# Optimization experiments

Measured on AMD Instinct MI355X. Metric: run time of the kernel, lower is better.

The kernel has to match this reference:

```python
import jax, jax.numpy as jnp
import numpy as np

B, L, CIN, COUT, HEADS = 8, 2048, 256, 256, 4
HD = COUT // HEADS
NEG_SLOPE = 0.2


def setup_inputs() -> dict:
    key = jax.random.key(0)
    k1, k2, k3, k4, k5 = jax.random.split(key, 5)
    x = jax.random.normal(k1, (B, L, CIN), dtype=jnp.float32)
    adj_mask = jax.random.randint(k2, (B, L, L), 0, 2) > 0  # bool [B,L,L]
    W = jax.random.normal(k3, (COUT, CIN), dtype=jnp.float32) * (1.0 / np.sqrt(CIN))
    att_src = jax.random.normal(k4, (1, HEADS, 1, HD), dtype=jnp.float32) * 0.1
    att_dst = jax.random.normal(k5, (1, HEADS, 1, HD), dtype=jnp.float32) * 0.1
    return {"x": x, "adj_mask": adj_mask, "W": W, "att_src": att_src, "att_dst": att_dst}


def reference(x, adj_mask, W, att_src, att_dst):
    Bb, Ll, _ = x.shape
    # linear projection (no bias), split heads: [B, H, L, D]
    h = jnp.einsum('blc,oc->blo', x, W).reshape(Bb, Ll, HEADS, HD).transpose(0, 2, 1, 3)
    # additive GAT scores
    a_src = jnp.sum(h * att_src, axis=-1, keepdims=True)          # [B,H,L,1]
    a_dst = jnp.sum(h * att_dst, axis=-1, keepdims=True)          # [B,H,L,1]
    e = a_src + jnp.swapaxes(a_dst, 2, 3)                          # [B,H,L,L]
    e = jnp.where(e >= 0, e, NEG_SLOPE * e)                        # leaky relu
    fill = jnp.finfo(e.dtype).min
    e = jnp.where(adj_mask[:, None, :, :], e, fill)                # mask non-edges
    alpha = jax.nn.softmax(e, axis=-1)                             # [B,H,L,L]
    # dropout is identity in eval/reference mode
    out = jnp.einsum('bhij,bhjd->bhid', alpha, h)                  # [B,H,L,D]
    return out.transpose(0, 2, 1, 3).reshape(Bb, Ll, COUT)
```

## Files before the change

kernel.cpp:

```cpp
#include <hip/hip_runtime.h>

#define B_ 8
#define L_ 2048
#define CIN_ 256
#define COUT_ 256
#define HEADS_ 4
#define HD_ 64
#define NEG_SLOPE_ 0.2f
#define LOG2E_ 1.4426950408889634f

#define TI 32
#define TJ 64
#define NJT (L_ / TJ)

typedef __attribute__((ext_vector_type(4))) float f32x4;
typedef __attribute__((ext_vector_type(8))) __bf16 bf16x8;
typedef __attribute__((ext_vector_type(4))) __bf16 bf16x4;


__global__ __launch_bounds__(256, 2)
void proj_kernel(const float* __restrict__ x, const float* __restrict__ W,
                 const float* __restrict__ att_src, const float* __restrict__ att_dst,
                 const int* __restrict__ adj, unsigned long long* __restrict__ abitsT,
                 __bf16* __restrict__ hF, float2* __restrict__ aE,
                 float2* __restrict__ aF) {
  __shared__ __align__(16) __bf16 Wl[COUT_][80];
  __shared__ __align__(16) __bf16 Al[2][2][512];

  const int tid = threadIdx.x;
  const int r0 = blockIdx.x * TI;
  const int b  = r0 >> 11;
  const int l0 = r0 & (L_ - 1);

  const int w = tid >> 6, lane = tid & 63, col = lane & 15, q = lane >> 4;
  const int si = tid >> 3, soct = tid & 7;
  const int wn = tid >> 2, wkq = tid & 3;

  {
    const size_t wid0 = (size_t)blockIdx.x * 256 + (size_t)w * 64;
    for (int c = 0; c < 64; ++c) {
      const size_t wid = wid0 + c;
      const int* p = adj + wid * 256 + lane;
      unsigned long long b0 = __ballot(p[0]   != 0);
      unsigned long long b1 = __ballot(p[64]  != 0);
      unsigned long long b2 = __ballot(p[128] != 0);
      unsigned long long b3 = __ballot(p[192] != 0);
      if (lane == 0) {
        const size_t row = wid >> 3;
        const int jw0 = (int)(wid & 7) * 4;
        const size_t bb = row >> 11, l = row & 2047;
        unsigned long long* dst = abitsT + (bb << 16) + l;
        dst[(size_t)(jw0 + 0) << 11] = b0;
        dst[(size_t)(jw0 + 1) << 11] = b1;
        dst[(size_t)(jw0 + 2) << 11] = b2;
        dst[(size_t)(jw0 + 3) << 11] = b3;
      }
    }
  }

  f32x4 acc[2][4];
#pragma unroll
  for (int mt = 0; mt < 2; ++mt)
#pragma unroll
    for (int nt = 0; nt < 4; ++nt) acc[mt][nt] = (f32x4)0.f;

  for (int kc = 0; kc < CIN_ / 64; ++kc) {
    __syncthreads();
#pragma unroll
    for (int rg = 0; rg < 4; ++rg) {
      const int row = rg * 64 + wn;
      const float4* ws = (const float4*)(W + (size_t)row * CIN_ + kc * 64 + wkq * 16);
#pragma unroll
      for (int u = 0; u < 4; ++u) {
        float4 f = ws[u];
        bf16x4 v;
        v[0] = (__bf16)f.x; v[1] = (__bf16)f.y; v[2] = (__bf16)f.z; v[3] = (__bf16)f.w;
        *(bf16x4*)&Wl[row][wkq * 16 + u * 4] = v;
      }
    }
    {
      const float4* xs = (const float4*)(x + (size_t)(r0 + si) * CIN_ + kc * 64 + soct * 8);
      float4 f0 = xs[0], f1 = xs[1];
      bf16x8 v;
      v[0] = (__bf16)f0.x; v[1] = (__bf16)f0.y; v[2] = (__bf16)f0.z; v[3] = (__bf16)f0.w;
      v[4] = (__bf16)f1.x; v[5] = (__bf16)f1.y; v[6] = (__bf16)f1.z; v[7] = (__bf16)f1.w;
      *(bf16x8*)&Al[si >> 4][soct >> 2][(((soct & 3) << 4) + (si & 15)) << 3] = v;
    }
    __syncthreads();

    bf16x8 af[2][2], bfr[2][4];
#pragma unroll
    for (int mt = 0; mt < 2; ++mt)
#pragma unroll
      for (int kt = 0; kt < 2; ++kt)
        af[mt][kt] = *(const bf16x8*)&Al[mt][kt][lane << 3];
#pragma unroll
    for (int kt = 0; kt < 2; ++kt)
#pragma unroll
      for (int nt = 0; nt < 4; ++nt)
        bfr[kt][nt] = *(const bf16x8*)&Wl[w * 64 + nt * 16 + col][kt * 32 + q * 8];
#pragma unroll
    for (int kt = 0; kt < 2; ++kt)
#pragma unroll
      for (int mt = 0; mt < 2; ++mt)
#pragma unroll
        for (int nt = 0; nt < 4; ++nt)
          acc[mt][nt] = __builtin_amdgcn_mfma_f32_16x16x32_bf16(
              af[mt][kt], bfr[kt][nt], acc[mt][nt], 0, 0, 0);
  }

  float asv[4], adv[4];
#pragma unroll
  for (int nt = 0; nt < 4; ++nt) {
    asv[nt] = att_src[w * 64 + nt * 16 + col];
    adv[nt] = att_dst[w * 64 + nt * 16 + col];
  }
#pragma unroll
  for (int mt = 0; mt < 2; ++mt)
#pragma unroll
    for (int reg = 0; reg < 4; ++reg) {
      float s = 0.f, d = 0.f;
#pragma unroll
      for (int nt = 0; nt < 4; ++nt) {
        s = fmaf(acc[mt][nt][reg], asv[nt], s);
        d = fmaf(acc[mt][nt][reg], adv[nt], d);
      }
      s += __shfl_xor(s, 1, 64); d += __shfl_xor(d, 1, 64);
      s += __shfl_xor(s, 2, 64); d += __shfl_xor(d, 2, 64);
      s += __shfl_xor(s, 4, 64); d += __shfl_xor(d, 4, 64);
      s += __shfl_xor(s, 8, 64); d += __shfl_xor(d, 8, 64);
      if (col == 0) {
        int il = mt * 16 + q * 4 + reg;
        const size_t idx = ((size_t)(b * HEADS_ + w) << 11) + l0 + il;
        float2 ev, fv;
        ev.x = __builtin_exp2f(s * LOG2E_);
        ev.y = __builtin_exp2f(s * (LOG2E_ * NEG_SLOPE_));
        fv.x = __builtin_exp2f(d * LOG2E_);
        fv.y = __builtin_exp2f(d * (LOG2E_ * NEG_SLOPE_));
        aE[idx] = ev;
        aF[idx] = fv;
      }
    }

  {
    const int jt_p = l0 >> 6;
    const int kt_p = (l0 >> 5) & 1;
    const int qhi = q >> 1, qlo = q & 1;
#pragma unroll
    for (int mt = 0; mt < 2; ++mt) {
      const int qp = mt * 2 + qhi;
#pragma unroll
      for (int nt = 0; nt < 4; ++nt) {
        bf16x4 v;
        v[0] = (__bf16)acc[mt][nt][0];
        v[1] = (__bf16)acc[mt][nt][1];
        v[2] = (__bf16)acc[mt][nt][2];
        v[3] = (__bf16)acc[mt][nt][3];
        const size_t off =
            ((((size_t)(b * HEADS_ + w) * 32 + jt_p) * 2 + kt_p) * 4 + nt) * 512 +
            (qp * 16 + col) * 8 + qlo * 4;
        *(bf16x4*)(hF + off) = v;
      }
    }
  }
}

__global__ __launch_bounds__(512, 4)
void attn_kernel(const __bf16* __restrict__ hF, const float2* __restrict__ aE,
                 const float2* __restrict__ aF,
                 const unsigned long long* __restrict__ abitsT,
                 float* __restrict__ out) {
  __shared__ __align__(16) float comb[HEADS_][64][40];

  const int tid = threadIdx.x;
  const int b  = blockIdx.x & 7;
  const int i0 = (blockIdx.x >> 3) * 32;

  const int w = tid >> 6, lane = tid & 63, col = lane & 15, q = lane >> 4;
  const int hh = w & 3;
  const int jh = w >> 2;
  const int jt0 = jh * (NJT / 2), jt1 = jt0 + NJT / 2;

  const size_t hl = (size_t)(b * HEADS_ + hh);
  const float2 EE[2] = {aE[(hl << 11) + i0 + col],
                        aE[(hl << 11) + i0 + 16 + col]};
  const float* afb = (const float*)(aF + (hl << 11)) + q * 16;
  const __bf16* hb = hF + hl * 131072 + lane * 8;
  const unsigned long long* mb = abitsT + ((size_t)b << 16) + i0 + col;

  bf16x8 bones;
#pragma unroll
  for (int e = 0; e < 8; ++e) bones[e] = (__bf16)1.0f;

  f32x4 acc[2][4], accl[2];
#pragma unroll
  for (int mt = 0; mt < 2; ++mt) {
    accl[mt] = (f32x4)0.f;
#pragma unroll
    for (int nt = 0; nt < 4; ++nt) acc[mt][nt] = (f32x4)0.f;
  }

  unsigned long long cm0 = mb[(size_t)jt0 << 11];
  unsigned long long cm1 = mb[((size_t)jt0 << 11) + 16];

  for (int jt = jt0; jt < jt1; ++jt) {
    bf16x8 cb[2][4];
#pragma unroll
    for (int kt = 0; kt < 2; ++kt)
#pragma unroll
      for (int nt = 0; nt < 4; ++nt)
        cb[kt][nt] = *(const bf16x8*)(hb + jt * 4096 + (kt * 4 + nt) * 512);
    float cf[2][16];
#pragma unroll
    for (int kt = 0; kt < 2; ++kt)
#pragma unroll
      for (int u = 0; u < 4; ++u)
        *(float4*)&cf[kt][u * 4] =
            *(const float4*)(afb + jt * 128 + kt * 64 + u * 4);

    const int jn = (jt < jt1 - 1) ? jt + 1 : jt;
    const unsigned long long nm0 = mb[(size_t)jn << 11];
    const unsigned long long nm1 = mb[((size_t)jn << 11) + 16];

    bf16x8 av[2][2];
#pragma unroll
    for (int mt = 0; mt < 2; ++mt) {
      const unsigned long long bw = mt ? cm1 : cm0;
      const float Ex = EE[mt].x, Ey = EE[mt].y;
#pragma unroll
      for (int kt = 0; kt < 2; ++kt) {
        const unsigned int tsh = ((unsigned int)(bw >> (kt * 32))) >> (q * 8);
#pragma unroll
        for (int e = 0; e < 8; ++e) {
          const float m1 = Ex * cf[kt][2 * e];
          const float m2 = Ey * cf[kt][2 * e + 1];
          const float pm = fmaxf(m1, m2);
          const float p = (tsh & (1u << e)) ? pm : 0.f;
          av[mt][kt][e] = (__bf16)p;
        }
      }
    }

#pragma unroll
    for (int kt = 0; kt < 2; ++kt)
#pragma unroll
      for (int mt = 0; mt < 2; ++mt) {
#pragma unroll
        for (int nt = 0; nt < 4; ++nt)
          acc[mt][nt] = __builtin_amdgcn_mfma_f32_16x16x32_bf16(
              av[mt][kt], cb[kt][nt], acc[mt][nt], 0, 0, 0);
        accl[mt] = __builtin_amdgcn_mfma_f32_16x16x32_bf16(
            av[mt][kt], bones, accl[mt], 0, 0, 0);
      }

    cm0 = nm0; cm1 = nm1;
  }

  if (jh == 1) {
#pragma unroll
    for (int mt = 0; mt < 2; ++mt)
#pragma unroll
      for (int nt = 0; nt < 4; ++nt)
        *(f32x4*)&comb[hh][lane][mt * 16 + nt * 4] = acc[mt][nt];
    *(f32x4*)&comb[hh][lane][32] = accl[0];
    *(f32x4*)&comb[hh][lane][36] = accl[1];
  }
  __syncthreads();
  if (jh == 0) {
#pragma unroll
    for (int mt = 0; mt < 2; ++mt) {
      const f32x4 lo = accl[mt] + *(const f32x4*)&comb[hh][lane][32 + mt * 4];
#pragma unroll
      for (int reg = 0; reg < 4; ++reg) {
        const int m = q * 4 + reg;
        const float linv = 1.0f / lo[reg];
        const size_t orow =
            ((size_t)(b * L_ + i0 + mt * 16 + m)) * COUT_ + hh * 64;
#pragma unroll
        for (int nt = 0; nt < 4; ++nt) {
          const float v =
              acc[mt][nt][reg] + comb[hh][lane][mt * 16 + nt * 4 + reg];
          out[orow + nt * 16 + col] = v * linv;
        }
      }
    }
  }
}

extern "C" void kernel_launch(void* const* d_in, const int* in_sizes, int n_in,
                              void* d_out, int out_size, void* d_ws, size_t ws_size,
                              hipStream_t stream) {
  const float* x       = (const float*)d_in[0];
  const int*   adj     = (const int*)d_in[1];
  const float* W       = (const float*)d_in[2];
  const float* att_src = (const float*)d_in[3];
  const float* att_dst = (const float*)d_in[4];
  float* out = (float*)d_out;

  char* ws = (char*)d_ws;
  __bf16* hF = (__bf16*)ws;
  float2* aE = (float2*)(ws + (8u << 20));
  float2* aF = (float2*)(ws + (9u << 20));
  unsigned long long* abitsT =
      (unsigned long long*)(ws + (10u << 20));

  proj_kernel<<<(B_ * L_) / TI, 256, 0, stream>>>(x, W, att_src, att_dst,
                                                  adj, abitsT, hF, aE, aF);
  attn_kernel<<<B_ * (L_ / 32), 512, 0, stream>>>(hF, aE, aF, abitsT, out);
}
```

Baseline: 324.9 us.

## Split adjacency bit-packing into its own kernel and restructure attention loop per k-slice

Moves the adjacency-to-bitmask ballot packing out of the projection kernel into a separate, fully parallel pack kernel with one wave per 256-int segment. Previously only 512 blocks each serially packed 64 segments per wave. The attention kernel now loads h and coefficient fragments per k-slice instead of for the whole tile, which lowers register pressure, and its occupancy hint in launch_bounds is dropped. This costs an extra kernel launch and may reduce the compiler's ability to overlap loads with MFMA work.

```diff
diff --git a/kernel.cpp b/kernel.cpp
--- a/kernel.cpp
+++ b/kernel.cpp
@@ -18,10 +18,30 @@
 typedef __attribute__((ext_vector_type(4))) __bf16 bf16x4;
 
 
+__global__ __launch_bounds__(256, 4)
+void pack_kernel(const int* __restrict__ adj, unsigned long long* __restrict__ abitsT) {
+  const size_t wid = ((size_t)blockIdx.x * 256 + threadIdx.x) >> 6;
+  const int lane = threadIdx.x & 63;
+  const int* p = adj + wid * 256 + lane;
+  unsigned long long b0 = __ballot(p[0]   != 0);
+  unsigned long long b1 = __ballot(p[64]  != 0);
+  unsigned long long b2 = __ballot(p[128] != 0);
+  unsigned long long b3 = __ballot(p[192] != 0);
+  if (lane == 0) {
+    const size_t row = wid >> 3;
+    const int jw0 = (int)(wid & 7) * 4;
+    const size_t bb = row >> 11, l = row & 2047;
+    unsigned long long* dst = abitsT + (bb << 16) + l;
+    dst[(size_t)(jw0 + 0) << 11] = b0;
+    dst[(size_t)(jw0 + 1) << 11] = b1;
+    dst[(size_t)(jw0 + 2) << 11] = b2;
+    dst[(size_t)(jw0 + 3) << 11] = b3;
+  }
+}
+
 __global__ __launch_bounds__(256, 2)
 void proj_kernel(const float* __restrict__ x, const float* __restrict__ W,
                  const float* __restrict__ att_src, const float* __restrict__ att_dst,
-                 const int* __restrict__ adj, unsigned long long* __restrict__ abitsT,
                  __bf16* __restrict__ hF, float2* __restrict__ aE,
                  float2* __restrict__ aF) {
   __shared__ __align__(16) __bf16 Wl[COUT_][80];
@@ -35,28 +55,6 @@
   const int w = tid >> 6, lane = tid & 63, col = lane & 15, q = lane >> 4;
   const int si = tid >> 3, soct = tid & 7;
   const int wn = tid >> 2, wkq = tid & 3;
-
-  {
-    const size_t wid0 = (size_t)blockIdx.x * 256 + (size_t)w * 64;
-    for (int c = 0; c < 64; ++c) {
-      const size_t wid = wid0 + c;
-      const int* p = adj + wid * 256 + lane;
-      unsigned long long b0 = __ballot(p[0]   != 0);
-      unsigned long long b1 = __ballot(p[64]  != 0);
-      unsigned long long b2 = __ballot(p[128] != 0);
-      unsigned long long b3 = __ballot(p[192] != 0);
-      if (lane == 0) {
-        const size_t row = wid >> 3;
-        const int jw0 = (int)(wid & 7) * 4;
-        const size_t bb = row >> 11, l = row & 2047;
-        unsigned long long* dst = abitsT + (bb << 16) + l;
-        dst[(size_t)(jw0 + 0) << 11] = b0;
-        dst[(size_t)(jw0 + 1) << 11] = b1;
-        dst[(size_t)(jw0 + 2) << 11] = b2;
-        dst[(size_t)(jw0 + 3) << 11] = b3;
-      }
-    }
-  }
 
   f32x4 acc[2][4];
 #pragma unroll
@@ -165,7 +163,7 @@
   }
 }
 
-__global__ __launch_bounds__(512, 4)
+__global__ __launch_bounds__(512)
 void attn_kernel(const __bf16* __restrict__ hF, const float2* __restrict__ aE,
                  const float2* __restrict__ aF,
                  const unsigned long long* __restrict__ abitsT,
@@ -204,54 +202,46 @@
   unsigned long long cm1 = mb[((size_t)jt0 << 11) + 16];
 
   for (int jt = jt0; jt < jt1; ++jt) {
-    bf16x8 cb[2][4];
-#pragma unroll
-    for (int kt = 0; kt < 2; ++kt)
-#pragma unroll
-      for (int nt = 0; nt < 4; ++nt)
-        cb[kt][nt] = *(const bf16x8*)(hb + jt * 4096 + (kt * 4 + nt) * 512);
-    float cf[2][16];
-#pragma unroll
-    for (int kt = 0; kt < 2; ++kt)
-#pragma unroll
-      for (int u = 0; u < 4; ++u)
-        *(float4*)&cf[kt][u * 4] =
-            *(const float4*)(afb + jt * 128 + kt * 64 + u * 4);
-
     const int jn = (jt < jt1 - 1) ? jt + 1 : jt;
     const unsigned long long nm0 = mb[(size_t)jn << 11];
     const unsigned long long nm1 = mb[((size_t)jn << 11) + 16];
 
-    bf16x8 av[2][2];
-#pragma unroll
-    for (int mt = 0; mt < 2; ++mt) {
-      const unsigned long long bw = mt ? cm1 : cm0;
-      const float Ex = EE[mt].x, Ey = EE[mt].y;
-#pragma unroll
-      for (int kt = 0; kt < 2; ++kt) {
+#pragma unroll
+    for (int kt = 0; kt < 2; ++kt) {
+      bf16x8 cb0 = *(const bf16x8*)(hb + jt * 4096 + (kt * 4 + 0) * 512);
+      bf16x8 cb1 = *(const bf16x8*)(hb + jt * 4096 + (kt * 4 + 1) * 512);
+      bf16x8 cb2 = *(const bf16x8*)(hb + jt * 4096 + (kt * 4 + 2) * 512);
+      bf16x8 cb3 = *(const bf16x8*)(hb + jt * 4096 + (kt * 4 + 3) * 512);
+      float cf[16];
+#pragma unroll
+      for (int u = 0; u < 4; ++u)
+        *(float4*)&cf[u * 4] =
+            *(const float4*)(afb + jt * 128 + kt * 64 + u * 4);
+
+      bf16x8 av[2];
+#pragma unroll
+      for (int mt = 0; mt < 2; ++mt) {
+        const unsigned long long bw = mt ? cm1 : cm0;
         const unsigned int tsh = ((unsigned int)(bw >> (kt * 32))) >> (q * 8);
+        const float Ex = EE[mt].x, Ey = EE[mt].y;
 #pragma unroll
         for (int e = 0; e < 8; ++e) {
-          const float m1 = Ex * cf[kt][2 * e];
-          const float m2 = Ey * cf[kt][2 * e + 1];
+          const float m1 = Ex * cf[2 * e];
+          const float m2 = Ey * cf[2 * e + 1];
           const float pm = fmaxf(m1, m2);
           const float p = (tsh & (1u << e)) ? pm : 0.f;
-          av[mt][kt][e] = (__bf16)p;
+          av[mt][e] = (__bf16)p;
         }
       }
-    }
-
-#pragma unroll
-    for (int kt = 0; kt < 2; ++kt)
 #pragma unroll
       for (int mt = 0; mt < 2; ++mt) {
-#pragma unroll
-        for (int nt = 0; nt < 4; ++nt)
-          acc[mt][nt] = __builtin_amdgcn_mfma_f32_16x16x32_bf16(
-              av[mt][kt], cb[kt][nt], acc[mt][nt], 0, 0, 0);
-        accl[mt] = __builtin_amdgcn_mfma_f32_16x16x32_bf16(
-            av[mt][kt], bones, accl[mt], 0, 0, 0);
-      }
+        acc[mt][0] = __builtin_amdgcn_mfma_f32_16x16x32_bf16(av[mt], cb0, acc[mt][0], 0, 0, 0);
+        acc[mt][1] = __builtin_amdgcn_mfma_f32_16x16x32_bf16(av[mt], cb1, acc[mt][1], 0, 0, 0);
+        acc[mt][2] = __builtin_amdgcn_mfma_f32_16x16x32_bf16(av[mt], cb2, acc[mt][2], 0, 0, 0);
+        acc[mt][3] = __builtin_amdgcn_mfma_f32_16x16x32_bf16(av[mt], cb3, acc[mt][3], 0, 0, 0);
+        accl[mt] = __builtin_amdgcn_mfma_f32_16x16x32_bf16(av[mt], bones, accl[mt], 0, 0, 0);
+      }
+    }
 
     cm0 = nm0; cm1 = nm1;
   }
@@ -304,7 +294,7 @@
   unsigned long long* abitsT =
       (unsigned long long*)(ws + (10u << 20));
 
-  proj_kernel<<<(B_ * L_) / TI, 256, 0, stream>>>(x, W, att_src, att_dst,
-                                                  adj, abitsT, hF, aE, aF);
+  pack_kernel<<<(B_ * L_ * (L_ / 256)) / 4, 256, 0, stream>>>(adj, abitsT);
+  proj_kernel<<<(B_ * L_) / TI, 256, 0, stream>>>(x, W, att_src, att_dst, hF, aE, aF);
   attn_kernel<<<B_ * (L_ / 32), 512, 0, stream>>>(hF, aE, aF, abitsT, out);
 }
```

Measured after the change: 261.1 us. 1.24x faster.
